# Kernel tuning notes

Measured on AMD Instinct MI355X. Metric: run time of the kernel, lower is better.

Reference implementation:

```python
import jax, jax.numpy as jnp
import numpy as np

S, U, NMEL, T = 32, 10, 40, 120
H, D = 768, 256


def setup_inputs() -> dict:
    key = jax.random.key(0)
    ks = jax.random.split(key, 16)
    def p(k, shape, scale=0.03):
        return jax.random.normal(k, shape, jnp.float32) * scale
    inp = {"mel": jax.random.normal(ks[0], (S, U, 1, NMEL, T), jnp.float32)}
    in_sizes = [NMEL, H, H]
    for l in range(3):
        inp[f"Wih{l}"] = p(ks[1 + 4 * l], (4 * H, in_sizes[l]))
        inp[f"Whh{l}"] = p(ks[2 + 4 * l], (4 * H, H))
        inp[f"bih{l}"] = p(ks[3 + 4 * l], (4 * H,))
        inp[f"bhh{l}"] = p(ks[4 + 4 * l], (4 * H,))
    inp["Wproj"] = p(ks[13], (D, H))
    inp["bproj"] = p(ks[14], (D,))
    inp["loss_w"] = jnp.array([10.0], jnp.float32)
    inp["loss_b"] = jnp.array([-5.0], jnp.float32)
    return inp


def _lstm_layer(x, Wih, Whh, bih, bhh):
    # x: (B, T, In) -> (B, T, H). PyTorch gate order: i, f, g, o.
    B = x.shape[0]
    Hh = Whh.shape[1]
    h0 = jnp.zeros((B, Hh), x.dtype)
    c0 = jnp.zeros((B, Hh), x.dtype)
    bias = bih + bhh
    def step(carry, xt):
        h, c = carry
        gates = xt @ Wih.T + h @ Whh.T + bias  # (B, 4H)
        i, f, g, o = jnp.split(gates, 4, axis=-1)
        c = jax.nn.sigmoid(f) * c + jax.nn.sigmoid(i) * jnp.tanh(g)
        h = jax.nn.sigmoid(o) * jnp.tanh(c)
        return (h, c), h
    _, hs = jax.lax.scan(step, (h0, c0), jnp.swapaxes(x, 0, 1))  # (T, B, H)
    return jnp.swapaxes(hs, 0, 1)


def _ge2e(d3, w, b):
    # d3: (S, U, D) unit-norm d-vectors; w, b: (1,) scalars.
    s, u, _ = d3.shape
    cent = d3.mean(axis=1)  # (S, D) per-speaker centroids
    # leave-one-out positive centroid: (U*cent - self) / (U-1)
    pos_cent = (cent[:, None, :] * u - d3) / (u - 1)  # (S, U, D)
    # cosine sim with eps=1e-6 (F.cosine_similarity clamps norms)
    na = jnp.maximum(jnp.linalg.norm(d3, axis=-1), 1e-6)
    npc = jnp.maximum(jnp.linalg.norm(pos_cent, axis=-1), 1e-6)
    pos_cos = jnp.sum(d3 * pos_cent, axis=-1) / (na * npc)  # (S, U)
    pos_sim = w[0] * pos_cos + b[0]
    # negative sims vs other speakers' centroids (eps=1e-8 default)
    nd = jnp.maximum(jnp.linalg.norm(d3, axis=-1), 1e-8)  # (S, U)
    nc = jnp.maximum(jnp.linalg.norm(cent, axis=-1), 1e-8)  # (S,)
    all_cos = jnp.einsum('sud,kd->suk', d3, cent) / (nd[..., None] * nc[None, None, :])
    jj = jnp.arange(s - 1)
    idx = jj[None, :] + (jj[None, :] >= jnp.arange(s)[:, None])  # (S, S-1), skips own speaker
    neg_cos = jnp.take_along_axis(all_cos, jnp.broadcast_to(idx[:, None, :], (s, u, s - 1)), axis=2)
    neg_sim = w[0] * neg_cos + b[0]
    # softmax GE2E loss: -pos + log sum exp(neg)
    loss = jnp.mean(-pos_sim + jax.scipy.special.logsumexp(neg_sim, axis=2))
    return loss, pos_sim.mean(), neg_sim.mean()


def reference(mel, Wih0, Whh0, bih0, bhh0, Wih1, Whh1, bih1, bhh1,
              Wih2, Whh2, bih2, bhh2, Wproj, bproj, loss_w, loss_b):
    s, u = mel.shape[0], mel.shape[1]
    x = mel.reshape(s * u, mel.shape[3], mel.shape[4])  # (B, 40, T)
    x = jnp.transpose(x, (0, 2, 1))  # (B, T, 40)
    for (Wih, Whh, bih, bhh) in ((Wih0, Whh0, bih0, bhh0),
                                 (Wih1, Whh1, bih1, bhh1),
                                 (Wih2, Whh2, bih2, bhh2)):
        x = _lstm_layer(x, Wih, Whh, bih, bhh)
    h = x[:, -1, :]  # last time step
    dvec = h @ Wproj.T + bproj
    dvec = dvec / jnp.linalg.norm(dvec, axis=1, keepdims=True)
    d3 = dvec.reshape(s, u, -1)
    return _ge2e(d3, loss_w, loss_b)
```

## Files before the change

### kernel.cpp

```cpp
#include <hip/hip_runtime.h>
#include <math.h>

#define S_    32
#define U_    10
#define B_    320
#define T_    120
#define NMEL_ 40
#define H_    768
#define G4_   3072
#define D_    256
#define XP_   64
#define K0_   (XP_ + H_)
#define K12_  (2 * H_)

#define NB0   48
#define NB12  96
#define NBLK  (NB0 + 2 * NB12)

#define SMEM_BYTES 159744

typedef _Float16 half8 __attribute__((ext_vector_type(8)));
typedef float floatx4 __attribute__((ext_vector_type(4)));

__device__ __forceinline__ float sigm(float x) {
  return 1.f / (1.f + __expf(-x));
}
__device__ __forceinline__ float tanh_f(float x) {
  x = fminf(15.f, fmaxf(-15.f, x));
  float e = __expf(2.f * x);
  return (e - 1.f) / (e + 1.f);
}

__device__ __forceinline__ void dma16(const void* g, void* l) {
  __builtin_amdgcn_global_load_lds(
      (const __attribute__((address_space(1))) unsigned int*)g,
      (__attribute__((address_space(3))) unsigned int*)l, 16, 0, 0);
}

template <int N>
__device__ __forceinline__ void waitvm() {
  __builtin_amdgcn_s_waitcnt(0x3FF0 | (N & 0xF) | ((N >> 4) << 14));
}


__global__ void prep_x0(const float* __restrict__ mel, _Float16* __restrict__ x0) {
  int idx = blockIdx.x * 256 + threadIdx.x;
  if (idx >= B_ * T_ * XP_) return;
  int k = idx & (XP_ - 1);
  int t = (idx >> 6) % T_;
  int b = idx / (XP_ * T_);
  float v = (k < NMEL_) ? mel[((size_t)b * NMEL_ + k) * T_ + t] : 0.f;
  x0[idx] = (_Float16)v;
}

__global__ void prep_w0(const float* __restrict__ Wih, const float* __restrict__ Whh,
                        _Float16* __restrict__ Wc) {
  int idx = blockIdx.x * 256 + threadIdx.x;
  if (idx >= G4_ * K0_) return;
  int k = idx % K0_;
  int n = idx / K0_;
  float v = 0.f;
  if (k < NMEL_)      v = Wih[(size_t)n * NMEL_ + k];
  else if (k >= XP_)  v = Whh[(size_t)n * H_ + (k - XP_)];
  Wc[idx] = (_Float16)v;
}

__global__ void prep_w12(const float* __restrict__ Wih, const float* __restrict__ Whh,
                         _Float16* __restrict__ Wc) {
  int idx = blockIdx.x * 256 + threadIdx.x;
  if (idx >= G4_ * K12_) return;
  int k = idx % K12_;
  int n = idx / K12_;
  float v = (k < H_) ? Wih[(size_t)n * H_ + k] : Whh[(size_t)n * H_ + (k - H_)];
  Wc[idx] = (_Float16)v;
}

__global__ void prep_bias(const float* __restrict__ bih, const float* __restrict__ bhh,
                          float* __restrict__ bias) {
  int idx = blockIdx.x * 256 + threadIdx.x;
  if (idx < G4_) bias[idx] = bih[idx] + bhh[idx];
}


__device__ __forceinline__ void wait_group(int* fl, int sp, int lp, int lane) {
  if (lp < 0 || lp > 2) return;
  if (sp < lp || sp > lp + T_ - 1) return;
  const int tgt = (lp == 0) ? NB0 : NB12;
  const int base = (sp * 3 + lp) * 96;
  int spin = 0;
  for (;;) {
    int v0 = (lane < tgt)
                 ? __hip_atomic_load(&fl[base + lane], __ATOMIC_RELAXED,
                                     __HIP_MEMORY_SCOPE_AGENT) : 1;
    int v1 = (lane + 64 < tgt)
                 ? __hip_atomic_load(&fl[base + 64 + lane], __ATOMIC_RELAXED,
                                     __HIP_MEMORY_SCOPE_AGENT) : 1;
    if (__all(v0 != 0 && v1 != 0)) break;
    __builtin_amdgcn_s_sleep(1);
    if (++spin > 2000000) break;
  }
}

template <int NT, int NSTG, int NC>
__device__ __forceinline__ void gemm_phase(
    const _Float16* __restrict__ lwW, int wchunk0, _Float16* __restrict__ lwA,
    const char* __restrict__ src, int strideE,
    int m0, int lane, floatx4 (&acc)[2][NT]) {
  const int lr = lane & 15, quad = lane >> 4;
  const int rrow = lane >> 2, rq = lane & 3;
  const int rqs = rq ^ ((rrow >> 1) & 3);
  const size_t o0 = ((size_t)(m0 + rrow) * strideE + rqs * 8) * 2;
  const size_t o1 = ((size_t)(m0 + 16 + rrow) * strideE + rqs * 8) * 2;

  auto issue = [&](int c) {
    const int slot = c % NSTG;
    char* ld = (char*)lwA + ((size_t)slot * 320 + m0) * 64;
    const char* g = src + (size_t)c * 64;
    dma16(g + o0, ld);
    dma16(g + o1, ld + 1024);
  };

#pragma unroll
  for (int p = 0; p < (NSTG < NC ? NSTG : NC); ++p) issue(p);

  const int asw = (quad ^ ((lr >> 1) & 3)) * 8;

#pragma unroll
  for (int c = 0; c < NC; ++c) {
    const int rem = NC - 1 - c;
    if (rem >= NSTG - 1)      waitvm<2 * (NSTG - 1)>();
    else if (rem == 1)        waitvm<2>();
    else                      waitvm<0>();
    const int slot = c % NSTG;
    const _Float16* aB = lwA + ((size_t)slot * 320 + m0 + lr) * 32 + asw;
    half8 a0 = *(const half8*)(aB);
    half8 a1 = *(const half8*)(aB + 16 * 32);
    half8 bf[NT];
#pragma unroll
    for (int nt = 0; nt < NT; ++nt)
      bf[nt] = *(const half8*)(lwW +
               ((size_t)((wchunk0 + c) * NT * 16 + nt * 16 + lr) * 32 + asw));
#pragma unroll
    for (int nt = 0; nt < NT; ++nt) {
      acc[0][nt] = __builtin_amdgcn_mfma_f32_16x16x32_f16(a0, bf[nt], acc[0][nt], 0, 0, 0);
      acc[1][nt] = __builtin_amdgcn_mfma_f32_16x16x32_f16(a1, bf[nt], acc[1][nt], 0, 0, 0);
    }
    if (c + NSTG < NC) issue(c + NSTG);
  }
}

__global__ __launch_bounds__(640)
void lstm_persist(const _Float16* __restrict__ x0,
                  const _Float16* __restrict__ Wc0, const _Float16* __restrict__ Wc1,
                  const _Float16* __restrict__ Wc2,
                  const float* __restrict__ bias, _Float16* __restrict__ hbuf,
                  int* __restrict__ flags) {
  extern __shared__ _Float16 lw[];
  const int bid = blockIdx.x;

  int layer, tile, units, K;
  const _Float16* Wsrc;
  if (bid < NB0)            { layer = 0; tile = bid;              units = 16; K = K0_;  Wsrc = Wc0; }
  else if (bid < NB0+NB12)  { layer = 1; tile = bid - NB0;        units = 8;  K = K12_; Wsrc = Wc1; }
  else                      { layer = 2; tile = bid - NB0 - NB12; units = 8;  K = K12_; Wsrc = Wc2; }
  const int nrows = units * 4;
  const int j0 = tile * units;
  _Float16* lwA = lw + (size_t)(K / 32) * nrows * 32;

  {
    const int total = (K / 32) * nrows * 4;
    for (int idx = threadIdx.x; idx < total; idx += 640) {
      int c = idx / (nrows * 4);
      int rem = idx % (nrows * 4);
      int r = rem >> 2;
      int q = rem & 3;
      int grow = (r / units) * H_ + j0 + (r % units);
      half8 v = *(const half8*)(Wsrc + (size_t)grow * K + c * 32 + q * 8);
      int qs = q ^ ((r >> 1) & 3);
      *(half8*)(lw + ((size_t)(c * nrows + r) * 32 + qs * 8)) = v;
    }
  }
  __syncthreads();

  const int lane = threadIdx.x & 63;
  const int wv = threadIdx.x >> 6;
  const int lr = lane & 15;
  const int quad = lane >> 4;
  const int m0 = wv * 32;
  const int m1 = wv * 32 + 16;
  const int j = j0 + ((units == 16) ? lr : (lr & 7));

  const float bI = bias[layer * G4_ + 0 * H_ + j];
  const float bF = bias[layer * G4_ + 1 * H_ + j];
  const float bG = bias[layer * G4_ + 2 * H_ + j];
  const float bO = bias[layer * G4_ + 3 * H_ + j];

  float cst[2][4] = {{0.f, 0.f, 0.f, 0.f}, {0.f, 0.f, 0.f, 0.f}};

  for (int t = 0; t < T_; ++t) {
    const int s = layer + t;
    const int pprev = (s - 1) & 1;
    const int pcur = s & 1;
    const _Float16* hown = hbuf + (size_t)(layer * 2 + pprev) * B_ * H_;
    _Float16* hout = hbuf + (size_t)(layer * 2 + pcur) * B_ * H_;

    floatx4 acc0[2][4];
    floatx4 acc2[2][2];

    if (layer == 0) {
#pragma unroll
      for (int a = 0; a < 2; ++a)
#pragma unroll
        for (int b = 0; b < 4; ++b) acc0[a][b] = (floatx4){0.f, 0.f, 0.f, 0.f};
      const char* xsrc = (const char*)(x0 + (size_t)t * XP_);
      gemm_phase<4, 2, 2>(lw, 0, lwA, xsrc, T_ * XP_, m0, lane, acc0);
      if (wv == 0) {
        wait_group(flags, s - 1, 0, lane);
        __builtin_amdgcn_fence(__ATOMIC_ACQUIRE, "agent");
      }
      __syncthreads();
      gemm_phase<4, 2, 24>(lw, 2, lwA, (const char*)hown, H_, m0, lane, acc0);
    } else {
      if (wv == 0) {
        wait_group(flags, s - 1, layer - 1, lane);
        __builtin_amdgcn_fence(__ATOMIC_ACQUIRE, "agent");
      }
      __syncthreads();
#pragma unroll
      for (int a = 0; a < 2; ++a)
#pragma unroll
        for (int b = 0; b < 2; ++b) acc2[a][b] = (floatx4){0.f, 0.f, 0.f, 0.f};
      const char* xsrc = (const char*)(hbuf + (size_t)((layer - 1) * 2 + pprev) * B_ * H_);
      gemm_phase<2, 3, 24>(lw, 0, lwA, xsrc, H_, m0, lane, acc2);
      wait_group(flags, s - 1, layer, lane);
      gemm_phase<2, 3, 24>(lw, 24, lwA, (const char*)hown, H_, m0, lane, acc2);
    }

    wait_group(flags, s - 1, layer + 1, lane);

    if (layer == 0) {
#pragma unroll
      for (int mt = 0; mt < 2; ++mt)
#pragma unroll
        for (int r = 0; r < 4; ++r) {
          float iv = acc0[mt][0][r] + bI;
          float fv = acc0[mt][1][r] + bF;
          float gv = acc0[mt][2][r] + bG;
          float ov = acc0[mt][3][r] + bO;
          float cn = sigm(fv) * cst[mt][r] + sigm(iv) * tanh_f(gv);
          cst[mt][r] = cn;
          int m = (mt ? m1 : m0) + quad * 4 + r;
          hout[(size_t)m * H_ + j] = (_Float16)(sigm(ov) * tanh_f(cn));
        }
    } else {
#pragma unroll
      for (int mt = 0; mt < 2; ++mt)
#pragma unroll
        for (int r = 0; r < 4; ++r) {
          float t0 = acc2[mt][0][r], t1 = acc2[mt][1][r];
          float p0 = __shfl_xor(t0, 8, 64);
          float p1 = __shfl_xor(t1, 8, 64);
          bool lo = (lr < 8);
          float iv = (lo ? t0 : p0) + bI;
          float fv = (lo ? p0 : t0) + bF;
          float gv = (lo ? t1 : p1) + bG;
          float ov = (lo ? p1 : t1) + bO;
          float cn = sigm(fv) * cst[mt][r] + sigm(iv) * tanh_f(gv);
          cst[mt][r] = cn;
          if (lo) {
            int m = (mt ? m1 : m0) + quad * 4 + r;
            hout[(size_t)m * H_ + j] = (_Float16)(sigm(ov) * tanh_f(cn));
          }
        }
    }

    __syncthreads();
    if (threadIdx.x == 0)
      __hip_atomic_store(&flags[(s * 3 + layer) * 96 + tile], 1, __ATOMIC_RELEASE,
                         __HIP_MEMORY_SCOPE_AGENT);
  }
}

__global__ void dvec_kernel(const _Float16* __restrict__ hlast, const float* __restrict__ Wproj,
                            const float* __restrict__ bproj, float* __restrict__ d3) {
  const int m = blockIdx.x;
  const int d = threadIdx.x;
  const _Float16* h = hlast + (size_t)m * H_;
  const float* w = Wproj + (size_t)d * H_;
  float acc = bproj[d];
  for (int k = 0; k < H_; k++) acc += (float)h[k] * w[k];
  __shared__ float red[256];
  red[d] = acc * acc;
  __syncthreads();
  for (int off = 128; off > 0; off >>= 1) {
    if (d < off) red[d] += red[d + off];
    __syncthreads();
  }
  float nrm = sqrtf(red[0]);
  d3[(size_t)m * D_ + d] = acc / nrm;
}

__device__ float block_reduce_sum(float x, float* red) {
  const int d = threadIdx.x;
  red[d] = x;
  __syncthreads();
  for (int off = 128; off > 0; off >>= 1) {
    if (d < off) red[d] += red[d + off];
    __syncthreads();
  }
  float r = red[0];
  __syncthreads();
  return r;
}

__global__ void cent_kernel(const float* __restrict__ d3, float* __restrict__ cent,
                            float* __restrict__ ncent) {
  const int sIdx = blockIdx.x;
  const int d = threadIdx.x;
  float acc = 0.f;
  for (int u = 0; u < U_; u++) acc += d3[((size_t)sIdx * U_ + u) * D_ + d];
  acc *= (1.f / U_);
  cent[sIdx * D_ + d] = acc;
  __shared__ float red[256];
  float n2 = block_reduce_sum(acc * acc, red);
  if (d == 0) ncent[sIdx] = fmaxf(sqrtf(n2), 1e-8f);
}

__global__ void ge2e_kernel(const float* __restrict__ d3, const float* __restrict__ cent,
                            const float* __restrict__ ncent, const float* __restrict__ loss_w,
                            const float* __restrict__ loss_b, float* __restrict__ accums) {
  const int p = blockIdx.x;
  const int sIdx = p / U_;
  const int d = threadIdx.x;
  __shared__ float red[256];
  __shared__ float sims[S_];

  const float v = d3[(size_t)p * D_ + d];
  const float cs = cent[sIdx * D_ + d];
  const float pc = (cs * U_ - v) * (1.f / (U_ - 1));

  float nv2 = block_reduce_sum(v * v, red);
  float npc2 = block_reduce_sum(pc * pc, red);
  float dotp = block_reduce_sum(v * pc, red);

  const float w = loss_w[0], b = loss_b[0];
  const float na = fmaxf(sqrtf(nv2), 1e-6f);
  const float npc = fmaxf(sqrtf(npc2), 1e-6f);
  const float pos_sim = w * (dotp / (na * npc)) + b;
  const float nd = fmaxf(sqrtf(nv2), 1e-8f);

  for (int k = 0; k < S_; k++) {
    float dk = block_reduce_sum(v * cent[k * D_ + d], red);
    if (d == 0) sims[k] = w * (dk / (nd * ncent[k])) + b;
  }
  __syncthreads();
  if (d == 0) {
    float mx = -1e30f;
    for (int k = 0; k < S_; k++)
      if (k != sIdx) mx = fmaxf(mx, sims[k]);
    float se = 0.f, sn = 0.f;
    for (int k = 0; k < S_; k++)
      if (k != sIdx) { se += expf(sims[k] - mx); sn += sims[k]; }
    float lse = mx + logf(se);
    atomicAdd(&accums[0], -pos_sim + lse);
    atomicAdd(&accums[1], pos_sim);
    atomicAdd(&accums[2], sn);
  }
}

__global__ void finalize_kernel(const float* __restrict__ accums, float* __restrict__ out) {
  if (threadIdx.x == 0) {
    out[0] = accums[0] / (float)(S_ * U_);
    out[1] = accums[1] / (float)(S_ * U_);
    out[2] = accums[2] / (float)(S_ * U_ * (S_ - 1));
  }
}

extern "C" void kernel_launch(void* const* d_in, const int* in_sizes, int n_in,
                              void* d_out, int out_size, void* d_ws, size_t ws_size,
                              hipStream_t stream) {
  const float* mel = (const float*)d_in[0];
  const float* Wih[3] = {(const float*)d_in[1], (const float*)d_in[5], (const float*)d_in[9]};
  const float* Whh[3] = {(const float*)d_in[2], (const float*)d_in[6], (const float*)d_in[10]};
  const float* bih[3] = {(const float*)d_in[3], (const float*)d_in[7], (const float*)d_in[11]};
  const float* bhh[3] = {(const float*)d_in[4], (const float*)d_in[8], (const float*)d_in[12]};
  const float* Wproj = (const float*)d_in[13];
  const float* bproj = (const float*)d_in[14];
  const float* loss_w = (const float*)d_in[15];
  const float* loss_b = (const float*)d_in[16];
  float* out = (float*)d_out;

  char* ws = (char*)d_ws;
  size_t off = 0;
  auto alloc = [&](size_t bytes) -> void* {
    void* p = ws + off;
    off = (off + bytes + 255) & ~(size_t)255;
    return p;
  };
  _Float16* x0   = (_Float16*)alloc((size_t)B_ * T_ * XP_ * 2);
  _Float16* Wc0  = (_Float16*)alloc((size_t)G4_ * K0_ * 2);
  _Float16* Wc1  = (_Float16*)alloc((size_t)G4_ * K12_ * 2);
  _Float16* Wc2  = (_Float16*)alloc((size_t)G4_ * K12_ * 2);
  float*    bias = (float*)alloc((size_t)3 * G4_ * 4);
  _Float16* hbuf = (_Float16*)alloc((size_t)6 * B_ * H_ * 2);
  float*    d3   = (float*)alloc((size_t)B_ * D_ * 4);
  float*    cent = (float*)alloc((size_t)S_ * D_ * 4);
  float*    ncent = (float*)alloc((size_t)S_ * 4);
  float*    accums = (float*)alloc(64);
  int*      flags = (int*)alloc((size_t)(T_ + 3) * 3 * 96 * 4);

  hipMemsetAsync(hbuf, 0, (size_t)6 * B_ * H_ * 2, stream);
  hipMemsetAsync(accums, 0, 64, stream);
  hipMemsetAsync(flags, 0, (size_t)(T_ + 3) * 3 * 96 * 4, stream);

  prep_x0<<<(B_ * T_ * XP_ + 255) / 256, 256, 0, stream>>>(mel, x0);
  prep_w0<<<(G4_ * K0_ + 255) / 256, 256, 0, stream>>>(Wih[0], Whh[0], Wc0);
  prep_w12<<<(G4_ * K12_ + 255) / 256, 256, 0, stream>>>(Wih[1], Whh[1], Wc1);
  prep_w12<<<(G4_ * K12_ + 255) / 256, 256, 0, stream>>>(Wih[2], Whh[2], Wc2);
  for (int l = 0; l < 3; l++)
    prep_bias<<<(G4_ + 255) / 256, 256, 0, stream>>>(bih[l], bhh[l], bias + l * G4_);

  hipFuncSetAttribute((const void*)lstm_persist,
                      hipFuncAttributeMaxDynamicSharedMemorySize, SMEM_BYTES);
  void* kargs[] = {(void*)&x0, (void*)&Wc0, (void*)&Wc1, (void*)&Wc2,
                   (void*)&bias, (void*)&hbuf, (void*)&flags};
  hipLaunchCooperativeKernel((const void*)lstm_persist, dim3(NBLK), dim3(640),
                             kargs, SMEM_BYTES, stream);

  const _Float16* hlast = hbuf + (size_t)(2 * 2 + 1) * B_ * H_;
  dvec_kernel<<<B_, 256, 0, stream>>>(hlast, Wproj, bproj, d3);
  cent_kernel<<<S_, 256, 0, stream>>>(d3, cent, ncent);
  ge2e_kernel<<<B_, 256, 0, stream>>>(d3, cent, ncent, loss_w, loss_b, accums);
  finalize_kernel<<<1, 64, 0, stream>>>(accums, out);
}
```

Measured before the change: 3.441 ms.

## Replace LDS DMA staging of activations with register-prefetched direct global loads

Activation tiles for the recurrent GEMM are now loaded directly from global memory into registers, using a small rotating prefetch buffer of depth 4 or 6, instead of being DMA-staged through LDS with global_load_lds and waitcnt. This frees the LDS staging area, so shared memory per block shrinks, and removes the explicit vmcnt management. The cost is more VGPR pressure and exposed global-load latency on each block's critical recurrent path. A workgroup acquire fence is added before reading the layer's own hidden state.

```diff
diff --git a/kernel.cpp b/kernel.cpp
--- a/kernel.cpp
+++ b/kernel.cpp
@@ -17,7 +17,7 @@
 #define NB12  96
 #define NBLK  (NB0 + 2 * NB12)
 
-#define SMEM_BYTES 159744
+#define SMEM_BYTES 106496
 
 typedef _Float16 half8 __attribute__((ext_vector_type(8)));
 typedef float floatx4 __attribute__((ext_vector_type(4)));
@@ -29,17 +29,6 @@
   x = fminf(15.f, fmaxf(-15.f, x));
   float e = __expf(2.f * x);
   return (e - 1.f) / (e + 1.f);
-}
-
-__device__ __forceinline__ void dma16(const void* g, void* l) {
-  __builtin_amdgcn_global_load_lds(
-      (const __attribute__((address_space(1))) unsigned int*)g,
-      (__attribute__((address_space(3))) unsigned int*)l, 16, 0, 0);
-}
-
-template <int N>
-__device__ __forceinline__ void waitvm() {
-  __builtin_amdgcn_s_waitcnt(0x3FF0 | (N & 0xF) | ((N >> 4) << 14));
 }
 
 
@@ -101,40 +90,28 @@
   }
 }
 
-template <int NT, int NSTG, int NC>
+template <int NT, int D, int NC>
 __device__ __forceinline__ void gemm_phase(
-    const _Float16* __restrict__ lwW, int wchunk0, _Float16* __restrict__ lwA,
-    const char* __restrict__ src, int strideE,
+    const _Float16* __restrict__ lwW, int wchunk0,
+    const _Float16* __restrict__ src, int strideE,
     int m0, int lane, floatx4 (&acc)[2][NT]) {
   const int lr = lane & 15, quad = lane >> 4;
-  const int rrow = lane >> 2, rq = lane & 3;
-  const int rqs = rq ^ ((rrow >> 1) & 3);
-  const size_t o0 = ((size_t)(m0 + rrow) * strideE + rqs * 8) * 2;
-  const size_t o1 = ((size_t)(m0 + 16 + rrow) * strideE + rqs * 8) * 2;
-
-  auto issue = [&](int c) {
-    const int slot = c % NSTG;
-    char* ld = (char*)lwA + ((size_t)slot * 320 + m0) * 64;
-    const char* g = src + (size_t)c * 64;
-    dma16(g + o0, ld);
-    dma16(g + o1, ld + 1024);
-  };
-
-#pragma unroll
-  for (int p = 0; p < (NSTG < NC ? NSTG : NC); ++p) issue(p);
-
+  const _Float16* a0p = src + (size_t)(m0 + lr) * strideE + quad * 8;
+  const _Float16* a1p = a0p + (size_t)16 * strideE;
   const int asw = (quad ^ ((lr >> 1) & 3)) * 8;
 
+  half8 abuf[(D < NC) ? D : NC][2];
+  constexpr int DD = (D < NC) ? D : NC;
+#pragma unroll
+  for (int p = 0; p < DD; ++p) {
+    abuf[p][0] = *(const half8*)(a0p + p * 32);
+    abuf[p][1] = *(const half8*)(a1p + p * 32);
+  }
+
 #pragma unroll
   for (int c = 0; c < NC; ++c) {
-    const int rem = NC - 1 - c;
-    if (rem >= NSTG - 1)      waitvm<2 * (NSTG - 1)>();
-    else if (rem == 1)        waitvm<2>();
-    else                      waitvm<0>();
-    const int slot = c % NSTG;
-    const _Float16* aB = lwA + ((size_t)slot * 320 + m0 + lr) * 32 + asw;
-    half8 a0 = *(const half8*)(aB);
-    half8 a1 = *(const half8*)(aB + 16 * 32);
+    half8 a0 = abuf[c % DD][0];
+    half8 a1 = abuf[c % DD][1];
     half8 bf[NT];
 #pragma unroll
     for (int nt = 0; nt < NT; ++nt)
@@ -145,7 +122,10 @@
       acc[0][nt] = __builtin_amdgcn_mfma_f32_16x16x32_f16(a0, bf[nt], acc[0][nt], 0, 0, 0);
       acc[1][nt] = __builtin_amdgcn_mfma_f32_16x16x32_f16(a1, bf[nt], acc[1][nt], 0, 0, 0);
     }
-    if (c + NSTG < NC) issue(c + NSTG);
+    if (c + DD < NC) {
+      abuf[c % DD][0] = *(const half8*)(a0p + (c + DD) * 32);
+      abuf[c % DD][1] = *(const half8*)(a1p + (c + DD) * 32);
+    }
   }
 }
 
@@ -165,7 +145,6 @@
   else                      { layer = 2; tile = bid - NB0 - NB12; units = 8;  K = K12_; Wsrc = Wc2; }
   const int nrows = units * 4;
   const int j0 = tile * units;
-  _Float16* lwA = lw + (size_t)(K / 32) * nrows * 32;
 
   {
     const int total = (K / 32) * nrows * 4;
@@ -212,14 +191,13 @@
       for (int a = 0; a < 2; ++a)
 #pragma unroll
         for (int b = 0; b < 4; ++b) acc0[a][b] = (floatx4){0.f, 0.f, 0.f, 0.f};
-      const char* xsrc = (const char*)(x0 + (size_t)t * XP_);
-      gemm_phase<4, 2, 2>(lw, 0, lwA, xsrc, T_ * XP_, m0, lane, acc0);
+      gemm_phase<4, 4, 2>(lw, 0, x0 + (size_t)t * XP_, T_ * XP_, m0, lane, acc0);
       if (wv == 0) {
         wait_group(flags, s - 1, 0, lane);
         __builtin_amdgcn_fence(__ATOMIC_ACQUIRE, "agent");
       }
       __syncthreads();
-      gemm_phase<4, 2, 24>(lw, 2, lwA, (const char*)hown, H_, m0, lane, acc0);
+      gemm_phase<4, 4, 24>(lw, 2, hown, H_, m0, lane, acc0);
     } else {
       if (wv == 0) {
         wait_group(flags, s - 1, layer - 1, lane);
@@ -230,10 +208,11 @@
       for (int a = 0; a < 2; ++a)
 #pragma unroll
         for (int b = 0; b < 2; ++b) acc2[a][b] = (floatx4){0.f, 0.f, 0.f, 0.f};
-      const char* xsrc = (const char*)(hbuf + (size_t)((layer - 1) * 2 + pprev) * B_ * H_);
-      gemm_phase<2, 3, 24>(lw, 0, lwA, xsrc, H_, m0, lane, acc2);
+      const _Float16* xsrc = hbuf + (size_t)((layer - 1) * 2 + pprev) * B_ * H_;
+      gemm_phase<2, 6, 24>(lw, 0, xsrc, H_, m0, lane, acc2);
       wait_group(flags, s - 1, layer, lane);
-      gemm_phase<2, 3, 24>(lw, 24, lwA, (const char*)hown, H_, m0, lane, acc2);
+      __builtin_amdgcn_fence(__ATOMIC_ACQUIRE, "workgroup");
+      gemm_phase<2, 6, 24>(lw, 24, hown, H_, m0, lane, acc2);
     }
 
     wait_group(flags, s - 1, layer + 1, lane);
```

New measurement: 5.214 ms. +51.5%, slower.

## Quad-buffer hidden states, relax WAR waits, add per-XCC leader acquire fence

Applied to the files above, without the earlier changes.

Expands the per-layer hidden-state ring from 2 to 4 buffers, so a block only waits for the next layer to finish step s-3 rather than s-1 before overwriting its output. Replaces the per-block wave-0 wait, acquire fence and __syncthreads with per-wave waits. It adds a per-XCC leader scheme in which the first block on each XCC per step issues the agent acquire fence and the others spin on a flag. The global->LDS DMA loads of hidden states now set the aux cache-policy bit. The goal is less serialization and fewer block-wide barriers in the persistent wavefront pipeline, at the cost of extra atomics and relying on a shared fence for cache coherence.

```diff
diff --git a/kernel.cpp b/kernel.cpp
--- a/kernel.cpp
+++ b/kernel.cpp
@@ -12,6 +12,7 @@
 #define XP_   64
 #define K0_   (XP_ + H_)
 #define K12_  (2 * H_)
+#define NP_   4
 
 #define NB0   48
 #define NB12  96
@@ -31,10 +32,11 @@
   return (e - 1.f) / (e + 1.f);
 }
 
+template <int AUX>
 __device__ __forceinline__ void dma16(const void* g, void* l) {
   __builtin_amdgcn_global_load_lds(
       (const __attribute__((address_space(1))) unsigned int*)g,
-      (__attribute__((address_space(3))) unsigned int*)l, 16, 0, 0);
+      (__attribute__((address_space(3))) unsigned int*)l, 16, 0, AUX);
 }
 
 template <int N>
@@ -101,7 +103,7 @@
   }
 }
 
-template <int NT, int NSTG, int NC>
+template <int NT, int NSTG, int NC, int AUX>
 __device__ __forceinline__ void gemm_phase(
     const _Float16* __restrict__ lwW, int wchunk0, _Float16* __restrict__ lwA,
     const char* __restrict__ src, int strideE,
@@ -116,8 +118,8 @@
     const int slot = c % NSTG;
     char* ld = (char*)lwA + ((size_t)slot * 320 + m0) * 64;
     const char* g = src + (size_t)c * 64;
-    dma16(g + o0, ld);
-    dma16(g + o1, ld + 1024);
+    dma16<AUX>(g + o0, ld);
+    dma16<AUX>(g + o1, ld + 1024);
   };
 
 #pragma unroll
@@ -154,7 +156,8 @@
                   const _Float16* __restrict__ Wc0, const _Float16* __restrict__ Wc1,
                   const _Float16* __restrict__ Wc2,
                   const float* __restrict__ bias, _Float16* __restrict__ hbuf,
-                  int* __restrict__ flags) {
+                  int* __restrict__ flags, int* __restrict__ tick,
+                  int* __restrict__ leadDone) {
   extern __shared__ _Float16 lw[];
   const int bid = blockIdx.x;
 
@@ -166,6 +169,10 @@
   const int nrows = units * 4;
   const int j0 = tile * units;
   _Float16* lwA = lw + (size_t)(K / 32) * nrows * 32;
+
+  unsigned xcc;
+  asm volatile("s_getreg_b32 %0, hwreg(HW_REG_XCC_ID)" : "=s"(xcc));
+  xcc &= 7;
 
   {
     const int total = (K / 32) * nrows * 4;
@@ -199,10 +206,27 @@
 
   for (int t = 0; t < T_; ++t) {
     const int s = layer + t;
-    const int pprev = (s - 1) & 1;
-    const int pcur = s & 1;
-    const _Float16* hown = hbuf + (size_t)(layer * 2 + pprev) * B_ * H_;
-    _Float16* hout = hbuf + (size_t)(layer * 2 + pcur) * B_ * H_;
+    const int pprev = (s - 1) & (NP_ - 1);
+    const int pcur = s & (NP_ - 1);
+    const _Float16* hown = hbuf + (size_t)(layer * NP_ + pprev) * B_ * H_;
+    _Float16* hout = hbuf + (size_t)(layer * NP_ + pcur) * B_ * H_;
+
+    if (threadIdx.x == 0) {
+      if (__hip_atomic_fetch_add(&tick[xcc * 128 + s], 1, __ATOMIC_RELAXED,
+                                 __HIP_MEMORY_SCOPE_AGENT) == 0) {
+        __builtin_amdgcn_fence(__ATOMIC_ACQUIRE, "agent");
+        __hip_atomic_store(&leadDone[xcc * 128 + s], 1, __ATOMIC_RELEASE,
+                           __HIP_MEMORY_SCOPE_AGENT);
+      }
+    }
+    if (lane == 0) {
+      int spin = 0;
+      while (__hip_atomic_load(&leadDone[xcc * 128 + s], __ATOMIC_RELAXED,
+                               __HIP_MEMORY_SCOPE_AGENT) == 0) {
+        __builtin_amdgcn_s_sleep(1);
+        if (++spin > 2000000) break;
+      }
+    }
 
     floatx4 acc0[2][4];
     floatx4 acc2[2][2];
@@ -213,30 +237,22 @@
 #pragma unroll
         for (int b = 0; b < 4; ++b) acc0[a][b] = (floatx4){0.f, 0.f, 0.f, 0.f};
       const char* xsrc = (const char*)(x0 + (size_t)t * XP_);
-      gemm_phase<4, 2, 2>(lw, 0, lwA, xsrc, T_ * XP_, m0, lane, acc0);
-      if (wv == 0) {
-        wait_group(flags, s - 1, 0, lane);
-        __builtin_amdgcn_fence(__ATOMIC_ACQUIRE, "agent");
-      }
-      __syncthreads();
-      gemm_phase<4, 2, 24>(lw, 2, lwA, (const char*)hown, H_, m0, lane, acc0);
+      gemm_phase<4, 2, 2, 0>(lw, 0, lwA, xsrc, T_ * XP_, m0, lane, acc0);
+      wait_group(flags, s - 1, 0, lane);
+      gemm_phase<4, 2, 24, 1>(lw, 2, lwA, (const char*)hown, H_, m0, lane, acc0);
     } else {
-      if (wv == 0) {
-        wait_group(flags, s - 1, layer - 1, lane);
-        __builtin_amdgcn_fence(__ATOMIC_ACQUIRE, "agent");
-      }
-      __syncthreads();
+      wait_group(flags, s - 1, layer - 1, lane);
 #pragma unroll
       for (int a = 0; a < 2; ++a)
 #pragma unroll
         for (int b = 0; b < 2; ++b) acc2[a][b] = (floatx4){0.f, 0.f, 0.f, 0.f};
-      const char* xsrc = (const char*)(hbuf + (size_t)((layer - 1) * 2 + pprev) * B_ * H_);
-      gemm_phase<2, 3, 24>(lw, 0, lwA, xsrc, H_, m0, lane, acc2);
+      const char* xsrc = (const char*)(hbuf + (size_t)((layer - 1) * NP_ + pprev) * B_ * H_);
+      gemm_phase<2, 3, 24, 1>(lw, 0, lwA, xsrc, H_, m0, lane, acc2);
       wait_group(flags, s - 1, layer, lane);
-      gemm_phase<2, 3, 24>(lw, 24, lwA, (const char*)hown, H_, m0, lane, acc2);
-    }
-
-    wait_group(flags, s - 1, layer + 1, lane);
+      gemm_phase<2, 3, 24, 1>(lw, 24, lwA, (const char*)hown, H_, m0, lane, acc2);
+    }
+
+    wait_group(flags, s - 3, layer + 1, lane);
 
     if (layer == 0) {
 #pragma unroll
@@ -402,16 +418,20 @@
   _Float16* Wc1  = (_Float16*)alloc((size_t)G4_ * K12_ * 2);
   _Float16* Wc2  = (_Float16*)alloc((size_t)G4_ * K12_ * 2);
   float*    bias = (float*)alloc((size_t)3 * G4_ * 4);
-  _Float16* hbuf = (_Float16*)alloc((size_t)6 * B_ * H_ * 2);
+  _Float16* hbuf = (_Float16*)alloc((size_t)3 * NP_ * B_ * H_ * 2);
   float*    d3   = (float*)alloc((size_t)B_ * D_ * 4);
   float*    cent = (float*)alloc((size_t)S_ * D_ * 4);
   float*    ncent = (float*)alloc((size_t)S_ * 4);
   float*    accums = (float*)alloc(64);
   int*      flags = (int*)alloc((size_t)(T_ + 3) * 3 * 96 * 4);
-
-  hipMemsetAsync(hbuf, 0, (size_t)6 * B_ * H_ * 2, stream);
+  int*      tick  = (int*)alloc((size_t)8 * 128 * 4);
+  int*      lead  = (int*)alloc((size_t)8 * 128 * 4);
+
+  hipMemsetAsync(hbuf, 0, (size_t)3 * NP_ * B_ * H_ * 2, stream);
   hipMemsetAsync(accums, 0, 64, stream);
   hipMemsetAsync(flags, 0, (size_t)(T_ + 3) * 3 * 96 * 4, stream);
+  hipMemsetAsync(tick, 0, (size_t)8 * 128 * 4, stream);
+  hipMemsetAsync(lead, 0, (size_t)8 * 128 * 4, stream);
 
   prep_x0<<<(B_ * T_ * XP_ + 255) / 256, 256, 0, stream>>>(mel, x0);
   prep_w0<<<(G4_ * K0_ + 255) / 256, 256, 0, stream>>>(Wih[0], Whh[0], Wc0);
@@ -423,11 +443,12 @@
   hipFuncSetAttribute((const void*)lstm_persist,
                       hipFuncAttributeMaxDynamicSharedMemorySize, SMEM_BYTES);
   void* kargs[] = {(void*)&x0, (void*)&Wc0, (void*)&Wc1, (void*)&Wc2,
-                   (void*)&bias, (void*)&hbuf, (void*)&flags};
+                   (void*)&bias, (void*)&hbuf, (void*)&flags, (void*)&tick,
+                   (void*)&lead};
   hipLaunchCooperativeKernel((const void*)lstm_persist, dim3(NBLK), dim3(640),
                              kargs, SMEM_BYTES, stream);
 
-  const _Float16* hlast = hbuf + (size_t)(2 * 2 + 1) * B_ * H_;
+  const _Float16* hlast = hbuf + (size_t)(2 * NP_ + 1) * B_ * H_;
   dvec_kernel<<<B_, 256, 0, stream>>>(hlast, Wproj, bproj, d3);
   cent_kernel<<<S_, 256, 0, stream>>>(d3, cent, ncent);
   ge2e_kernel<<<B_, 256, 0, stream>>>(d3, cent, ncent, loss_w, loss_b, accums);
```

Result: faster. 3.341 ms (-2.9%).
